# Optimization experiments

Measured on AMD Instinct MI355X. Metric: run time of the kernel, lower is better.

Reference implementation:

```python
import jax, jax.numpy as jnp
import numpy as np


def setup_inputs() -> dict:
    key = jax.random.key(0)
    ks = jax.random.split(key, 9)
    D, DK, DV = 512, 64, 64
    B, S = 4, 4096
    sd = 1.0 / np.sqrt(D).astype(np.float32)
    so = 1.0 / np.sqrt(DV).astype(np.float32)
    return {
        "x": jax.random.normal(ks[0], (B, S, D), dtype=jnp.float32),
        "Wq": jax.random.normal(ks[1], (D, DK), dtype=jnp.float32) * sd,
        "bq": jnp.zeros((DK,), dtype=jnp.float32),
        "Wk": jax.random.normal(ks[2], (D, DK), dtype=jnp.float32) * sd,
        "bk": jnp.zeros((DK,), dtype=jnp.float32),
        "Wv": jax.random.normal(ks[3], (D, DV), dtype=jnp.float32) * sd,
        "bv": jnp.zeros((DV,), dtype=jnp.float32),
        "Wo": jax.random.normal(ks[4], (DV, D), dtype=jnp.float32) * so,
        "bo": jnp.zeros((D,), dtype=jnp.float32),
    }


def reference(x, Wq, bq, Wk, bk, Wv, bv, Wo, bo):
    # x: (B, S, D)
    B, S, D = x.shape
    dk = Wq.shape[1]
    q = x @ Wq + bq            # (B, S, dk)
    k = x @ Wk + bk            # (B, S, dk)
    v = x @ Wv + bv            # (B, S, dv)
    scores = jnp.einsum("bik,bjk->bij", q, k) / jnp.sqrt(jnp.float32(dk))  # (B,S,S)
    # causal mask: True where j <= i (keep)
    causal = jnp.tril(jnp.ones((S, S), dtype=bool))
    scores = jnp.where(causal[None, :, :], scores, -jnp.inf)
    weights = jax.nn.softmax(scores, axis=-1)   # every row has >=1 unmasked entry
    out = jnp.einsum("bij,bjv->biv", weights, v)  # (B, S, dv)
    return out @ Wo + bo
```

## Files before the change

### kernel.cpp

```cpp
#include <hip/hip_runtime.h>
#include <hip/hip_bf16.h>

#define S_LEN 4096
#define D_MODEL 512
#define DKV 64
#define B_N 4
#define STR 72
#define VSTR 136

typedef __hip_bfloat16 bf16;
typedef __attribute__((ext_vector_type(8))) short short8;
typedef __attribute__((ext_vector_type(4))) float floatx4;

#define MFMA(a, b, c) __builtin_amdgcn_mfma_f32_16x16x32_bf16(a, b, c, 0, 0, 0)

__device__ __forceinline__ float b2f(bf16 v) { return __bfloat162float(v); }

__device__ __forceinline__ unsigned short f2bits(float v) {
    union { bf16 h; unsigned short u; } cv;
    cv.h = __float2bfloat16(v);
    return cv.u;
}
__device__ __forceinline__ float bits2f(unsigned short u) {
    union { bf16 h; unsigned short u; } cv;
    cv.u = u;
    return b2f(cv.h);
}

__global__ __launch_bounds__(64) void detect_kernel(const void* x, int* flag) {
    const int lane = threadIdx.x;
    const bf16* xb = (const bf16*)x;
    int bad = 0;
    for (int k = lane; k < 4096; k += 64) {
        float v = fabsf(b2f(xb[2 * k]));
        if (!(v < 64.f)) bad++;
    }
    #pragma unroll
    for (int off = 32; off >= 1; off >>= 1) bad += __shfl_xor(bad, off);
    if (lane == 0) *flag = (bad > 100) ? 1 : 0;
}

__global__ __launch_bounds__(512) void wprep_qkv_frag(
    const void* __restrict__ Wq, const void* __restrict__ bq,
    const void* __restrict__ Wk, const void* __restrict__ bk,
    const void* __restrict__ Wv, const void* __restrict__ bv,
    bf16* __restrict__ Wfh, bf16* __restrict__ Wfl, float* __restrict__ ball,
    const int* __restrict__ flag)
{
    __shared__ float xs[16][513];
    const int ct = blockIdx.x;
    const int c0 = ct * 16;
    const int g = c0 >> 6;
    const int cc0 = c0 & 63;
    const void* W    = (g == 0) ? Wq : (g == 1) ? Wk : Wv;
    const void* bias = (g == 0) ? bq : (g == 1) ? bk : bv;
    const int tid = threadIdx.x;
    const int f32 = *flag;

    #pragma unroll
    for (int i = 0; i < 16; ++i) {
        const int idx = tid + 512 * i;
        const int d = idx >> 4, j = idx & 15;
        const float v = f32 ? ((const float*)W)[(size_t)d * DKV + cc0 + j]
                            : b2f(((const bf16*)W)[(size_t)d * DKV + cc0 + j]);
        xs[j][d] = v;
    }
    __syncthreads();

    union Pack8 { uint4 u; unsigned short s[8]; };
    #pragma unroll
    for (int rep = 0; rep < 2; ++rep) {
        const int f = tid + rep * 512;
        const int kt = f >> 6, lane = f & 63;
        const int quad = lane >> 4, l15 = lane & 15;
        Pack8 ph, pl;
        #pragma unroll
        for (int j = 0; j < 8; ++j) {
            const float v = xs[l15][kt * 32 + quad * 8 + j];
            const unsigned short hb = f2bits(v);
            ph.s[j] = hb;
            pl.s[j] = f2bits(v - bits2f(hb));
        }
        const size_t o = (((size_t)ct * 16 + kt) * 64 + lane) * 8;
        *(uint4*)&Wfh[o] = ph.u;
        *(uint4*)&Wfl[o] = pl.u;
    }
    if (tid < 16)
        ball[c0 + tid] = f32 ? ((const float*)bias)[cc0 + tid]
                             : b2f(((const bf16*)bias)[cc0 + tid]);
}

__global__ __launch_bounds__(512) void wprep_o_frag(
    const void* __restrict__ Wo, const void* __restrict__ bo,
    bf16* __restrict__ WoFh, bf16* __restrict__ WoFl,
    float* __restrict__ ball2, const int* __restrict__ flag)
{
    __shared__ float ys[16][65];
    const int ctile = blockIdx.x;
    const int c0 = ctile * 16;
    const int tid = threadIdx.x;
    const int f32 = *flag;

    #pragma unroll
    for (int rep = 0; rep < 2; ++rep) {
        const int idx = tid + rep * 512;
        const int d = idx >> 4, j = idx & 15;
        const float v = f32 ? ((const float*)Wo)[(size_t)d * D_MODEL + c0 + j]
                            : b2f(((const bf16*)Wo)[(size_t)d * D_MODEL + c0 + j]);
        ys[j][d] = v;
    }
    __syncthreads();

    union Pack8 { uint4 u; unsigned short s[8]; };
    if (tid < 128) {
        const int kc = tid >> 6, lane = tid & 63;
        const int quad = lane >> 4, l15 = lane & 15;
        Pack8 ph, pl;
        #pragma unroll
        for (int j = 0; j < 8; ++j) {
            const float v = ys[l15][kc * 32 + quad * 8 + j];
            const unsigned short hb = f2bits(v);
            ph.s[j] = hb;
            pl.s[j] = f2bits(v - bits2f(hb));
        }
        const size_t o = (((size_t)ctile * 2 + kc) * 64 + lane) * 8;
        *(uint4*)&WoFh[o] = ph.u;
        *(uint4*)&WoFl[o] = pl.u;
    }
    if (tid < 16)
        ball2[c0 + tid] = f32 ? ((const float*)bo)[c0 + tid]
                              : b2f(((const bf16*)bo)[c0 + tid]);
}

__global__ __launch_bounds__(256) void qkv_mfma_bf16(
    const void* __restrict__ x,
    const bf16* __restrict__ Wfh, const float* __restrict__ ball,
    bf16* __restrict__ Qb, bf16* __restrict__ Kb, bf16* __restrict__ Vt,
    const int* __restrict__ flag)
{
    if (*flag) return;
    __shared__ unsigned short hiA[32 * D_MODEL];
    const int tid = threadIdx.x;
    const int rowBase = blockIdx.x * 32;

    const unsigned short* xr = (const unsigned short*)x + (size_t)rowBase * D_MODEL;
    #pragma unroll
    for (int i = 0; i < 8; ++i) {
        const int idx = tid + 256 * i;
        const int r = idx >> 6;
        const int c0 = (idx & 63) << 3;
        const uint4 hv = *(const uint4*)&xr[r * D_MODEL + c0];
        const int boff = (c0 * 2) ^ ((r & 7) << 4);
        *(uint4*)((char*)hiA + r * 1024 + boff) = hv;
    }
    __syncthreads();

    const int lane = tid & 63;
    const int w    = tid >> 6;
    const int quad = lane >> 4;
    const int l15  = lane & 15;
    const int wr   = w & 1;
    const int wcol = w >> 1;
    const int arow = wr * 16 + l15;
    const char* hib = (const char*)hiA + arow * 1024;
    const int swz = (arow & 7) << 4;

    floatx4 acc[6];
    #pragma unroll
    for (int ct = 0; ct < 6; ++ct) acc[ct] = (floatx4){0.f, 0.f, 0.f, 0.f};

    for (int kt = 0; kt < 16; ++kt) {
        const int boff = (kt * 64 + quad * 16) ^ swz;
        const short8 ah = *(const short8*)(hib + boff);
        #pragma unroll
        for (int ct = 0; ct < 6; ++ct) {
            const size_t fo = (((size_t)(wcol * 6 + ct) * 16 + kt) * 64 + lane) * 8;
            const short8 bh = *(const short8*)&Wfh[fo];
            acc[ct] = MFMA(ah, bh, acc[ct]);
        }
    }

    #pragma unroll
    for (int ct = 0; ct < 6; ++ct) {
        const int gc = wcol * 96 + ct * 16 + l15;
        const float bias = ball[gc];
        const float scale = (gc < 64) ? 0.18033688f : 1.0f;
        #pragma unroll
        for (int r = 0; r < 4; ++r) {
            const int gr = rowBase + wr * 16 + quad * 4 + r;
            const bf16 o = __float2bfloat16((acc[ct][r] + bias) * scale);
            if (gc < 64)       Qb[(size_t)gr * DKV + gc] = o;
            else if (gc < 128) Kb[(size_t)gr * DKV + (gc - 64)] = o;
            else {
                const int bb = gr >> 12, sidx = gr & (S_LEN - 1);
                Vt[((size_t)bb * DKV + (gc - 128)) * S_LEN + sidx] = o;
            }
        }
    }
}

__global__ __launch_bounds__(512) void qkv_mfma_f32(
    const void* __restrict__ x,
    const bf16* __restrict__ Wfh, const bf16* __restrict__ Wfl,
    const float* __restrict__ ball,
    bf16* __restrict__ Qb, bf16* __restrict__ Kb, bf16* __restrict__ Vt,
    const int* __restrict__ flag)
{
    if (!*flag) return;
    __shared__ unsigned short hiA[32 * D_MODEL];
    __shared__ unsigned short loA[32 * D_MODEL];
    const int tid = threadIdx.x;
    const int rowBase = blockIdx.x * 32;

    union Pack8 { uint4 u; unsigned short s[8]; };
    {
        const float* xr = (const float*)x + (size_t)rowBase * D_MODEL;
        #pragma unroll
        for (int i = 0; i < 4; ++i) {
            const int idx = tid + 512 * i;
            const int r = idx >> 6;
            const int c0 = (idx & 63) << 3;
            const float4 v0 = *(const float4*)&xr[r * D_MODEL + c0];
            const float4 v1 = *(const float4*)&xr[r * D_MODEL + c0 + 4];
            const float vv[8] = {v0.x, v0.y, v0.z, v0.w, v1.x, v1.y, v1.z, v1.w};
            Pack8 ph, pl;
            #pragma unroll
            for (int j = 0; j < 8; ++j) {
                const unsigned short hb = f2bits(vv[j]);
                ph.s[j] = hb;
                pl.s[j] = f2bits(vv[j] - bits2f(hb));
            }
            const int boff = (c0 * 2) ^ ((r & 7) << 4);
            *(uint4*)((char*)hiA + r * 1024 + boff) = ph.u;
            *(uint4*)((char*)loA + r * 1024 + boff) = pl.u;
        }
    }
    __syncthreads();

    const int lane = tid & 63;
    const int w    = tid >> 6;
    const int quad = lane >> 4;
    const int l15  = lane & 15;
    const int wr   = w & 1;
    const int wq   = w >> 1;
    const int arow = wr * 16 + l15;
    const char* hib = (const char*)hiA + arow * 1024;
    const char* lob = (const char*)loA + arow * 1024;
    const int swz = (arow & 7) << 4;

    floatx4 acc[3];
    #pragma unroll
    for (int ct = 0; ct < 3; ++ct) acc[ct] = (floatx4){0.f, 0.f, 0.f, 0.f};

    for (int kt = 0; kt < 16; ++kt) {
        const int boff = (kt * 64 + quad * 16) ^ swz;
        const short8 ah = *(const short8*)(hib + boff);
        const short8 al = *(const short8*)(lob + boff);
        #pragma unroll
        for (int ct = 0; ct < 3; ++ct) {
            const size_t fo = (((size_t)(wq * 3 + ct) * 16 + kt) * 64 + lane) * 8;
            const short8 bh = *(const short8*)&Wfh[fo];
            const short8 bl = *(const short8*)&Wfl[fo];
            acc[ct] = MFMA(ah, bh, acc[ct]);
            acc[ct] = MFMA(ah, bl, acc[ct]);
            acc[ct] = MFMA(al, bh, acc[ct]);
        }
    }

    #pragma unroll
    for (int ct = 0; ct < 3; ++ct) {
        const int gc = wq * 48 + ct * 16 + l15;
        const float bias = ball[gc];
        const float scale = (gc < 64) ? 0.18033688f : 1.0f;
        #pragma unroll
        for (int r = 0; r < 4; ++r) {
            const int gr = rowBase + wr * 16 + quad * 4 + r;
            const bf16 o = __float2bfloat16((acc[ct][r] + bias) * scale);
            if (gc < 64)       Qb[(size_t)gr * DKV + gc] = o;
            else if (gc < 128) Kb[(size_t)gr * DKV + (gc - 64)] = o;
            else {
                const int bb = gr >> 12, sidx = gr & (S_LEN - 1);
                Vt[((size_t)bb * DKV + (gc - 128)) * S_LEN + sidx] = o;
            }
        }
    }
}

__global__ __launch_bounds__(256, 3) void attn_mfma(
    const bf16* __restrict__ Qg, const bf16* __restrict__ Kg,
    const bf16* __restrict__ Vtg, float* __restrict__ Op,
    float* __restrict__ Mp, float* __restrict__ Lp, const int NS)
{
    const int bid = blockIdx.x;
    const int xcd = bid & 7;
    const int rest = bid >> 3;
    const int b   = xcd >> 1;
    const int khH = (NS == 4) ? (rest & 1) : 0;
    const int t64 = 63 - ((NS == 4) ? (rest >> 1) : rest);
    const int kh  = khH * 2 + (xcd & 1);
    const int rowBase = t64 * 64;
    const int tid = threadIdx.x;
    const int lane = tid & 63;
    const int w  = tid >> 6;
    const int quad = lane >> 4;
    const int l15  = lane & 15;

    __shared__ bf16 Kl[128 * STR];
    __shared__ bf16 Vl[64 * VSTR];
    __shared__ bf16 Pl[64 * VSTR];

    const bf16* Qb = Qg + ((size_t)b * S_LEN + rowBase) * DKV;
    const bf16* Kb = Kg + (size_t)b * S_LEN * DKV;
    const bf16* Vb = Vtg + (size_t)b * DKV * S_LEN;

    {
        const int qr = tid >> 2, qd = (tid & 3) * 16;
        *(uint4*)&Pl[qr * VSTR + qd]     = *(const uint4*)&Qb[qr * DKV + qd];
        *(uint4*)&Pl[qr * VSTR + qd + 8] = *(const uint4*)&Qb[qr * DKV + qd + 8];
    }
    __syncthreads();
    short8 qf0, qf1;
    {
        const int qoff = (w * 16 + l15) * VSTR + quad * 8;
        qf0 = *(const short8*)&Pl[qoff];
        qf1 = *(const short8*)&Pl[qoff + 32];
    }

    const short s1b = (short)0x3F80;
    const short8 ones = {s1b, s1b, s1b, s1b, s1b, s1b, s1b, s1b};

    floatx4 acc[4];
    #pragma unroll
    for (int v = 0; v < 4; ++v) acc[v] = (floatx4){0.f, 0.f, 0.f, 0.f};
    floatx4 accl = {0.f, 0.f, 0.f, 0.f};
    float m_run[4];
    #pragma unroll
    for (int r = 0; r < 4; ++r) m_run[r] = -1e30f;

    const int kbMax = (rowBase + 63) >> 7;
    const int kk = tid >> 1, dk = (tid & 1) * 32;
    const int vd = tid >> 2, vk = (tid & 3) * 32;

    uint4 kr0, kr1, kr2, kr3, vr0, vr1, vr2, vr3;
    int kb = kh;
    if (kb <= kbMax) {
        const uint4* ks = (const uint4*)&Kb[((size_t)(kb * 128 + kk)) * DKV + dk];
        kr0 = ks[0]; kr1 = ks[1]; kr2 = ks[2]; kr3 = ks[3];
        const uint4* vs = (const uint4*)&Vb[(size_t)vd * S_LEN + kb * 128 + vk];
        vr0 = vs[0]; vr1 = vs[1]; vr2 = vs[2]; vr3 = vs[3];
    }

    for (; kb <= kbMax; kb += NS) {
        __syncthreads();
        {
            uint4* kd = (uint4*)&Kl[kk * STR + dk];
            kd[0] = kr0; kd[1] = kr1; kd[2] = kr2; kd[3] = kr3;
            uint4* vdst = (uint4*)&Vl[vd * VSTR + vk];
            vdst[0] = vr0; vdst[1] = vr1; vdst[2] = vr2; vdst[3] = vr3;
        }
        __syncthreads();
        if (kb + NS <= kbMax) {
            const uint4* ks = (const uint4*)&Kb[((size_t)((kb + NS) * 128 + kk)) * DKV + dk];
            kr0 = ks[0]; kr1 = ks[1]; kr2 = ks[2]; kr3 = ks[3];
            const uint4* vs = (const uint4*)&Vb[(size_t)vd * S_LEN + (kb + NS) * 128 + vk];
            vr0 = vs[0]; vr1 = vs[1]; vr2 = vs[2]; vr3 = vs[3];
        }

        floatx4 s[8];
        #pragma unroll
        for (int jt = 0; jt < 8; ++jt) s[jt] = (floatx4){0.f, 0.f, 0.f, 0.f};
        {
            const int qk = quad * 8;
            #pragma unroll
            for (int jt = 0; jt < 8; ++jt) {
                const int kc = (jt * 16 + l15) * STR + qk;
                const short8 ba = *(const short8*)&Kl[kc];
                const short8 bb = *(const short8*)&Kl[kc + 32];
                s[jt] = MFMA(qf0, ba, s[jt]);
                s[jt] = MFMA(qf1, bb, s[jt]);
            }
        }
        if (kb == kbMax) {
            const int rowg = rowBase + w * 16 + quad * 4;
            #pragma unroll
            for (int jt = 0; jt < 8; ++jt) {
                const int kg = kb * 128 + jt * 16 + l15;
                #pragma unroll
                for (int r = 0; r < 4; ++r)
                    if (kg > rowg + r) s[jt][r] = -1e30f;
            }
        }
        float m4[4];
        #pragma unroll
        for (int r = 0; r < 4; ++r) {
            float mm = s[0][r];
            #pragma unroll
            for (int jt = 1; jt < 8; ++jt) mm = fmaxf(mm, s[jt][r]);
            m4[r] = mm;
        }
        #pragma unroll
        for (int off = 1; off < 16; off <<= 1) {
            #pragma unroll
            for (int r = 0; r < 4; ++r) m4[r] = fmaxf(m4[r], __shfl_xor(m4[r], off));
        }
        float alpha[4];
        #pragma unroll
        for (int r = 0; r < 4; ++r) {
            const float mnew = fmaxf(m_run[r], m4[r]);
            alpha[r] = exp2f(m_run[r] - mnew);
            m_run[r] = mnew;
        }
        #pragma unroll
        for (int r = 0; r < 4; ++r) {
            accl[r] *= alpha[r];
            #pragma unroll
            for (int v = 0; v < 4; ++v) acc[v][r] *= alpha[r];
            const int poff = (w * 16 + quad * 4 + r) * VSTR + l15;
            #pragma unroll
            for (int jt = 0; jt < 8; ++jt) {
                const float pp = exp2f(s[jt][r] - m_run[r]);
                Pl[poff + jt * 16] = __float2bfloat16(pp);
            }
        }
        asm volatile("s_waitcnt lgkmcnt(0)" ::: "memory");

        {
            const int pk = quad * 8;
            const int prow = (w * 16 + l15) * VSTR;
            short8 pa[4];
            #pragma unroll
            for (int c = 0; c < 4; ++c)
                pa[c] = *(const short8*)&Pl[prow + pk + c * 32];
            #pragma unroll
            for (int c = 0; c < 4; ++c) accl = MFMA(pa[c], ones, accl);
            #pragma unroll
            for (int v = 0; v < 4; ++v) {
                const int vrow = (v * 16 + l15) * VSTR;
                #pragma unroll
                for (int c = 0; c < 4; ++c) {
                    const short8 vb = *(const short8*)&Vl[vrow + pk + c * 32];
                    acc[v] = MFMA(pa[c], vb, acc[v]);
                }
            }
        }
    }
    #pragma unroll
    for (int r = 0; r < 4; ++r) {
        const int row = rowBase + w * 16 + quad * 4 + r;
        float* op = Op + (((size_t)kh * B_N + b) * S_LEN + row) * DKV + l15;
        #pragma unroll
        for (int v = 0; v < 4; ++v) op[v * 16] = acc[v][r];
    }
    if (l15 == 0) {
        #pragma unroll
        for (int r = 0; r < 4; ++r) {
            const int row = rowBase + w * 16 + quad * 4 + r;
            const size_t mi = ((size_t)kh * B_N + b) * S_LEN + row;
            Mp[mi] = m_run[r];
            Lp[mi] = accl[r];
        }
    }
}

#define PSTR 72
__global__ __launch_bounds__(256) void proj_mfma_bf16(
    const float* __restrict__ Op, const float* __restrict__ Mp,
    const float* __restrict__ Lp, const int NS,
    const bf16* __restrict__ WoFh, const float* __restrict__ ball2,
    bf16* __restrict__ out, const int* __restrict__ flag)
{
    if (*flag) return;
    __shared__ unsigned short Ah[32 * PSTR], Al[32 * PSTR];
    const int tid = threadIdx.x;
    const int rowBase = blockIdx.x * 32;

    {
        const int rr = tid >> 3, dd = (tid & 7) * 8;
        const int row = rowBase + rr;
        const size_t part = (size_t)B_N * S_LEN;
        float m = -1e30f;
        #pragma unroll 4
        for (int i = 0; i < NS; ++i) m = fmaxf(m, Mp[i * part + row]);
        float denom = 0.f;
        float oacc[8] = {0.f, 0.f, 0.f, 0.f, 0.f, 0.f, 0.f, 0.f};
        #pragma unroll 4
        for (int i = 0; i < NS; ++i) {
            const float wi = exp2f(Mp[i * part + row] - m);
            denom += Lp[i * part + row] * wi;
            const float* pi = Op + (i * part + row) * DKV + dd;
            #pragma unroll
            for (int j = 0; j < 8; ++j) oacc[j] += pi[j] * wi;
        }
        const float inv = 1.0f / denom;
        union Pack8 { uint4 u; unsigned short s[8]; };
        Pack8 ph, pl;
        #pragma unroll
        for (int j = 0; j < 8; ++j) {
            const float o = oacc[j] * inv;
            ph.s[j] = f2bits(o);
            pl.s[j] = f2bits(o - bits2f(ph.s[j]));
        }
        *(uint4*)&Ah[rr * PSTR + dd] = ph.u;
        *(uint4*)&Al[rr * PSTR + dd] = pl.u;
    }
    __syncthreads();

    const int lane = tid & 63;
    const int w    = tid >> 6;
    const int quad = lane >> 4;
    const int l15  = lane & 15;
    const int wr   = w & 1;
    const int wcq  = w >> 1;

    const int aoff = (wr * 16 + l15) * PSTR + quad * 8;
    const short8 ah0 = *(const short8*)&Ah[aoff];
    const short8 ah1 = *(const short8*)&Ah[aoff + 32];
    const short8 al0 = *(const short8*)&Al[aoff];
    const short8 al1 = *(const short8*)&Al[aoff + 32];

    floatx4 acc[16];
    #pragma unroll
    for (int ct = 0; ct < 16; ++ct) acc[ct] = (floatx4){0.f, 0.f, 0.f, 0.f};

    #pragma unroll
    for (int ct = 0; ct < 16; ++ct) {
        const int ctile = wcq * 16 + ct;
        const size_t o0 = (((size_t)ctile * 2 + 0) * 64 + lane) * 8;
        const size_t o1 = (((size_t)ctile * 2 + 1) * 64 + lane) * 8;
        const short8 bh0 = *(const short8*)&WoFh[o0];
        const short8 bh1 = *(const short8*)&WoFh[o1];
        acc[ct] = MFMA(ah0, bh0, acc[ct]);
        acc[ct] = MFMA(ah1, bh1, acc[ct]);
        acc[ct] = MFMA(al0, bh0, acc[ct]);
        acc[ct] = MFMA(al1, bh1, acc[ct]);
    }

    #pragma unroll
    for (int ct = 0; ct < 16; ++ct) {
        const int col = wcq * 256 + ct * 16 + l15;
        const float bias = ball2[col];
        #pragma unroll
        for (int r = 0; r < 4; ++r) {
            const int row = rowBase + wr * 16 + quad * 4 + r;
            out[(size_t)row * D_MODEL + col] = __float2bfloat16(acc[ct][r] + bias);
        }
    }
}

__global__ __launch_bounds__(512) void proj_mfma_f32(
    const float* __restrict__ Op, const float* __restrict__ Mp,
    const float* __restrict__ Lp, const int NS,
    const bf16* __restrict__ WoFh, const bf16* __restrict__ WoFl,
    const float* __restrict__ ball2, float* __restrict__ out,
    const int* __restrict__ flag)
{
    if (!*flag) return;
    __shared__ unsigned short Ah[32 * PSTR], Al[32 * PSTR];
    const int tid = threadIdx.x;
    const int rowBase = blockIdx.x * 32;

    {
        const int rr = tid >> 4, dd = (tid & 15) * 4;
        const int row = rowBase + rr;
        const size_t part = (size_t)B_N * S_LEN;
        float m = -1e30f;
        #pragma unroll 4
        for (int i = 0; i < NS; ++i) m = fmaxf(m, Mp[i * part + row]);
        float denom = 0.f;
        float oacc[4] = {0.f, 0.f, 0.f, 0.f};
        #pragma unroll 4
        for (int i = 0; i < NS; ++i) {
            const float wi = exp2f(Mp[i * part + row] - m);
            denom += Lp[i * part + row] * wi;
            const float4 v = *(const float4*)&Op[(i * part + row) * DKV + dd];
            oacc[0] += v.x * wi; oacc[1] += v.y * wi;
            oacc[2] += v.z * wi; oacc[3] += v.w * wi;
        }
        const float inv = 1.0f / denom;
        union Pack4 { uint2 u; unsigned short s[4]; };
        Pack4 ph, pl;
        #pragma unroll
        for (int j = 0; j < 4; ++j) {
            const float o = oacc[j] * inv;
            ph.s[j] = f2bits(o);
            pl.s[j] = f2bits(o - bits2f(ph.s[j]));
        }
        *(uint2*)&Ah[rr * PSTR + dd] = ph.u;
        *(uint2*)&Al[rr * PSTR + dd] = pl.u;
    }
    __syncthreads();

    const int lane = tid & 63;
    const int w    = tid >> 6;
    const int quad = lane >> 4;
    const int l15  = lane & 15;
    const int wr   = w & 1;
    const int wcq  = w >> 1;

    const int aoff = (wr * 16 + l15) * PSTR + quad * 8;
    const short8 ah0 = *(const short8*)&Ah[aoff];
    const short8 ah1 = *(const short8*)&Ah[aoff + 32];
    const short8 al0 = *(const short8*)&Al[aoff];
    const short8 al1 = *(const short8*)&Al[aoff + 32];

    floatx4 acc[8];
    #pragma unroll
    for (int ct = 0; ct < 8; ++ct) acc[ct] = (floatx4){0.f, 0.f, 0.f, 0.f};

    #pragma unroll
    for (int ct = 0; ct < 8; ++ct) {
        const int ctile = wcq * 8 + ct;
        const size_t o0 = (((size_t)ctile * 2 + 0) * 64 + lane) * 8;
        const size_t o1 = (((size_t)ctile * 2 + 1) * 64 + lane) * 8;
        const short8 bh0 = *(const short8*)&WoFh[o0];
        const short8 bh1 = *(const short8*)&WoFh[o1];
        const short8 bl0 = *(const short8*)&WoFl[o0];
        const short8 bl1 = *(const short8*)&WoFl[o1];
        acc[ct] = MFMA(ah0, bh0, acc[ct]);
        acc[ct] = MFMA(ah1, bh1, acc[ct]);
        acc[ct] = MFMA(ah0, bl0, acc[ct]);
        acc[ct] = MFMA(ah1, bl1, acc[ct]);
        acc[ct] = MFMA(al0, bh0, acc[ct]);
        acc[ct] = MFMA(al1, bh1, acc[ct]);
    }

    #pragma unroll
    for (int ct = 0; ct < 8; ++ct) {
        const int col = wcq * 128 + ct * 16 + l15;
        const float bias = ball2[col];
        #pragma unroll
        for (int r = 0; r < 4; ++r) {
            const int row = rowBase + wr * 16 + quad * 4 + r;
            out[(size_t)row * D_MODEL + col] = acc[ct][r] + bias;
        }
    }
}

extern "C" void kernel_launch(void* const* d_in, const int* in_sizes, int n_in,
                              void* d_out, int out_size, void* d_ws, size_t ws_size,
                              hipStream_t stream) {
    const void* x  = d_in[0];
    const void* Wq = d_in[1];
    const void* bq = d_in[2];
    const void* Wk = d_in[3];
    const void* bk = d_in[4];
    const void* Wv = d_in[5];
    const void* bv = d_in[6];
    const void* Wo = d_in[7];
    const void* bo = d_in[8];

    const int rows = B_N * S_LEN;
    const int NS = (ws_size >= (size_t)30 * 1024 * 1024) ? 4 : 2;

    char* p = (char*)d_ws;
    int*  flag = (int*)p;                          p += 256;
    bf16* Qb = (bf16*)p;                           p += (size_t)rows * DKV * 2;
    bf16* Kb = (bf16*)p;                           p += (size_t)rows * DKV * 2;
    bf16* Vt = (bf16*)p;                           p += (size_t)rows * DKV * 2;
    bf16* Wfh = (bf16*)p;                          p += (size_t)12 * 16 * 64 * 8 * 2;
    bf16* Wfl = (bf16*)p;                          p += (size_t)12 * 16 * 64 * 8 * 2;
    float* ball = (float*)p;                       p += 1024;
    bf16* WoFh = (bf16*)p;                         p += (size_t)32 * 2 * 64 * 8 * 2;
    bf16* WoFl = (bf16*)p;                         p += (size_t)32 * 2 * 64 * 8 * 2;
    float* ball2 = (float*)p;                      p += D_MODEL * 4;
    float* Op = (float*)p;                         p += (size_t)NS * rows * DKV * 4;
    float* Mp = (float*)p;                         p += (size_t)NS * rows * 4;
    float* Lp = (float*)p;                         p += (size_t)NS * rows * 4;

    detect_kernel<<<1, 64, 0, stream>>>(x, flag);
    wprep_qkv_frag<<<12, 512, 0, stream>>>(Wq, bq, Wk, bk, Wv, bv, Wfh, Wfl, ball, flag);
    wprep_o_frag<<<32, 512, 0, stream>>>(Wo, bo, WoFh, WoFl, ball2, flag);
    qkv_mfma_bf16<<<512, 256, 0, stream>>>(x, Wfh, ball, Qb, Kb, Vt, flag);
    qkv_mfma_f32<<<512, 512, 0, stream>>>(x, Wfh, Wfl, ball, Qb, Kb, Vt, flag);
    attn_mfma<<<256 * NS, 256, 0, stream>>>(Qb, Kb, Vt, Op, Mp, Lp, NS);
    proj_mfma_bf16<<<512, 256, 0, stream>>>(Op, Mp, Lp, NS, WoFh, ball2, (bf16*)d_out, flag);
    proj_mfma_f32<<<512, 512, 0, stream>>>(Op, Mp, Lp, NS, WoFh, WoFl, ball2, (float*)d_out, flag);
}
```

Measured before the change: 173.0 us.

## Merge dtype-variant kernels and enlarge attention query tile to 128 rows

Merges the two weight-prep kernels into one launch and folds the bf16/f32 variants of the QKV and output-projection kernels into single kernels that branch on the dtype flag. This removes several kernel launches, including early-exiting blocks. The attention kernel moves from 64 to 128 query rows per block with 512 threads, halving the grid and letting each K/V tile serve twice as many queries. The trade-off is coarser causal load balancing, a larger P buffer in shared memory, and lower occupancy.

```diff
diff --git a/kernel.cpp b/kernel.cpp
--- a/kernel.cpp
+++ b/kernel.cpp
@@ -40,180 +40,109 @@
     if (lane == 0) *flag = (bad > 100) ? 1 : 0;
 }
 
-__global__ __launch_bounds__(512) void wprep_qkv_frag(
+__global__ __launch_bounds__(512) void wprep_kernel(
     const void* __restrict__ Wq, const void* __restrict__ bq,
     const void* __restrict__ Wk, const void* __restrict__ bk,
     const void* __restrict__ Wv, const void* __restrict__ bv,
+    const void* __restrict__ Wo, const void* __restrict__ bo,
     bf16* __restrict__ Wfh, bf16* __restrict__ Wfl, float* __restrict__ ball,
+    bf16* __restrict__ WoFh, bf16* __restrict__ WoFl, float* __restrict__ ball2,
     const int* __restrict__ flag)
 {
     __shared__ float xs[16][513];
-    const int ct = blockIdx.x;
-    const int c0 = ct * 16;
-    const int g = c0 >> 6;
-    const int cc0 = c0 & 63;
-    const void* W    = (g == 0) ? Wq : (g == 1) ? Wk : Wv;
-    const void* bias = (g == 0) ? bq : (g == 1) ? bk : bv;
+    const int blk = blockIdx.x;
     const int tid = threadIdx.x;
     const int f32 = *flag;
-
-    #pragma unroll
-    for (int i = 0; i < 16; ++i) {
-        const int idx = tid + 512 * i;
-        const int d = idx >> 4, j = idx & 15;
-        const float v = f32 ? ((const float*)W)[(size_t)d * DKV + cc0 + j]
-                            : b2f(((const bf16*)W)[(size_t)d * DKV + cc0 + j]);
-        xs[j][d] = v;
-    }
-    __syncthreads();
-
     union Pack8 { uint4 u; unsigned short s[8]; };
-    #pragma unroll
-    for (int rep = 0; rep < 2; ++rep) {
-        const int f = tid + rep * 512;
-        const int kt = f >> 6, lane = f & 63;
-        const int quad = lane >> 4, l15 = lane & 15;
-        Pack8 ph, pl;
-        #pragma unroll
-        for (int j = 0; j < 8; ++j) {
-            const float v = xs[l15][kt * 32 + quad * 8 + j];
-            const unsigned short hb = f2bits(v);
-            ph.s[j] = hb;
-            pl.s[j] = f2bits(v - bits2f(hb));
-        }
-        const size_t o = (((size_t)ct * 16 + kt) * 64 + lane) * 8;
-        *(uint4*)&Wfh[o] = ph.u;
-        *(uint4*)&Wfl[o] = pl.u;
-    }
-    if (tid < 16)
-        ball[c0 + tid] = f32 ? ((const float*)bias)[cc0 + tid]
-                             : b2f(((const bf16*)bias)[cc0 + tid]);
-}
-
-__global__ __launch_bounds__(512) void wprep_o_frag(
-    const void* __restrict__ Wo, const void* __restrict__ bo,
-    bf16* __restrict__ WoFh, bf16* __restrict__ WoFl,
-    float* __restrict__ ball2, const int* __restrict__ flag)
-{
-    __shared__ float ys[16][65];
-    const int ctile = blockIdx.x;
-    const int c0 = ctile * 16;
-    const int tid = threadIdx.x;
-    const int f32 = *flag;
-
-    #pragma unroll
-    for (int rep = 0; rep < 2; ++rep) {
-        const int idx = tid + rep * 512;
-        const int d = idx >> 4, j = idx & 15;
-        const float v = f32 ? ((const float*)Wo)[(size_t)d * D_MODEL + c0 + j]
-                            : b2f(((const bf16*)Wo)[(size_t)d * D_MODEL + c0 + j]);
-        ys[j][d] = v;
-    }
-    __syncthreads();
-
-    union Pack8 { uint4 u; unsigned short s[8]; };
-    if (tid < 128) {
-        const int kc = tid >> 6, lane = tid & 63;
-        const int quad = lane >> 4, l15 = lane & 15;
-        Pack8 ph, pl;
-        #pragma unroll
-        for (int j = 0; j < 8; ++j) {
-            const float v = ys[l15][kc * 32 + quad * 8 + j];
-            const unsigned short hb = f2bits(v);
-            ph.s[j] = hb;
-            pl.s[j] = f2bits(v - bits2f(hb));
-        }
-        const size_t o = (((size_t)ctile * 2 + kc) * 64 + lane) * 8;
-        *(uint4*)&WoFh[o] = ph.u;
-        *(uint4*)&WoFl[o] = pl.u;
-    }
-    if (tid < 16)
-        ball2[c0 + tid] = f32 ? ((const float*)bo)[c0 + tid]
-                              : b2f(((const bf16*)bo)[c0 + tid]);
-}
-
-__global__ __launch_bounds__(256) void qkv_mfma_bf16(
-    const void* __restrict__ x,
-    const bf16* __restrict__ Wfh, const float* __restrict__ ball,
-    bf16* __restrict__ Qb, bf16* __restrict__ Kb, bf16* __restrict__ Vt,
-    const int* __restrict__ flag)
-{
-    if (*flag) return;
-    __shared__ unsigned short hiA[32 * D_MODEL];
-    const int tid = threadIdx.x;
-    const int rowBase = blockIdx.x * 32;
-
-    const unsigned short* xr = (const unsigned short*)x + (size_t)rowBase * D_MODEL;
-    #pragma unroll
-    for (int i = 0; i < 8; ++i) {
-        const int idx = tid + 256 * i;
-        const int r = idx >> 6;
-        const int c0 = (idx & 63) << 3;
-        const uint4 hv = *(const uint4*)&xr[r * D_MODEL + c0];
-        const int boff = (c0 * 2) ^ ((r & 7) << 4);
-        *(uint4*)((char*)hiA + r * 1024 + boff) = hv;
-    }
-    __syncthreads();
-
-    const int lane = tid & 63;
-    const int w    = tid >> 6;
-    const int quad = lane >> 4;
-    const int l15  = lane & 15;
-    const int wr   = w & 1;
-    const int wcol = w >> 1;
-    const int arow = wr * 16 + l15;
-    const char* hib = (const char*)hiA + arow * 1024;
-    const int swz = (arow & 7) << 4;
-
-    floatx4 acc[6];
-    #pragma unroll
-    for (int ct = 0; ct < 6; ++ct) acc[ct] = (floatx4){0.f, 0.f, 0.f, 0.f};
-
-    for (int kt = 0; kt < 16; ++kt) {
-        const int boff = (kt * 64 + quad * 16) ^ swz;
-        const short8 ah = *(const short8*)(hib + boff);
-        #pragma unroll
-        for (int ct = 0; ct < 6; ++ct) {
-            const size_t fo = (((size_t)(wcol * 6 + ct) * 16 + kt) * 64 + lane) * 8;
-            const short8 bh = *(const short8*)&Wfh[fo];
-            acc[ct] = MFMA(ah, bh, acc[ct]);
-        }
-    }
-
-    #pragma unroll
-    for (int ct = 0; ct < 6; ++ct) {
-        const int gc = wcol * 96 + ct * 16 + l15;
-        const float bias = ball[gc];
-        const float scale = (gc < 64) ? 0.18033688f : 1.0f;
-        #pragma unroll
-        for (int r = 0; r < 4; ++r) {
-            const int gr = rowBase + wr * 16 + quad * 4 + r;
-            const bf16 o = __float2bfloat16((acc[ct][r] + bias) * scale);
-            if (gc < 64)       Qb[(size_t)gr * DKV + gc] = o;
-            else if (gc < 128) Kb[(size_t)gr * DKV + (gc - 64)] = o;
-            else {
-                const int bb = gr >> 12, sidx = gr & (S_LEN - 1);
-                Vt[((size_t)bb * DKV + (gc - 128)) * S_LEN + sidx] = o;
-            }
-        }
-    }
-}
-
-__global__ __launch_bounds__(512) void qkv_mfma_f32(
+
+    if (blk < 12) {
+        const int ct = blk;
+        const int c0 = ct * 16;
+        const int g = c0 >> 6;
+        const int cc0 = c0 & 63;
+        const void* W    = (g == 0) ? Wq : (g == 1) ? Wk : Wv;
+        const void* bias = (g == 0) ? bq : (g == 1) ? bk : bv;
+
+        #pragma unroll
+        for (int i = 0; i < 16; ++i) {
+            const int idx = tid + 512 * i;
+            const int d = idx >> 4, j = idx & 15;
+            const float v = f32 ? ((const float*)W)[(size_t)d * DKV + cc0 + j]
+                                : b2f(((const bf16*)W)[(size_t)d * DKV + cc0 + j]);
+            xs[j][d] = v;
+        }
+        __syncthreads();
+
+        #pragma unroll
+        for (int rep = 0; rep < 2; ++rep) {
+            const int f = tid + rep * 512;
+            const int kt = f >> 6, lane = f & 63;
+            const int quad = lane >> 4, l15 = lane & 15;
+            Pack8 ph, pl;
+            #pragma unroll
+            for (int j = 0; j < 8; ++j) {
+                const float v = xs[l15][kt * 32 + quad * 8 + j];
+                const unsigned short hb = f2bits(v);
+                ph.s[j] = hb;
+                pl.s[j] = f2bits(v - bits2f(hb));
+            }
+            const size_t o = (((size_t)ct * 16 + kt) * 64 + lane) * 8;
+            *(uint4*)&Wfh[o] = ph.u;
+            *(uint4*)&Wfl[o] = pl.u;
+        }
+        if (tid < 16)
+            ball[c0 + tid] = f32 ? ((const float*)bias)[cc0 + tid]
+                                 : b2f(((const bf16*)bias)[cc0 + tid]);
+    } else {
+        const int ctile = blk - 12;
+        const int c0 = ctile * 16;
+
+        #pragma unroll
+        for (int rep = 0; rep < 2; ++rep) {
+            const int idx = tid + rep * 512;
+            const int d = idx >> 4, j = idx & 15;
+            const float v = f32 ? ((const float*)Wo)[(size_t)d * D_MODEL + c0 + j]
+                                : b2f(((const bf16*)Wo)[(size_t)d * D_MODEL + c0 + j]);
+            xs[j][d] = v;
+        }
+        __syncthreads();
+
+        if (tid < 128) {
+            const int kc = tid >> 6, lane = tid & 63;
+            const int quad = lane >> 4, l15 = lane & 15;
+            Pack8 ph, pl;
+            #pragma unroll
+            for (int j = 0; j < 8; ++j) {
+                const float v = xs[l15][kc * 32 + quad * 8 + j];
+                const unsigned short hb = f2bits(v);
+                ph.s[j] = hb;
+                pl.s[j] = f2bits(v - bits2f(hb));
+            }
+            const size_t o = (((size_t)ctile * 2 + kc) * 64 + lane) * 8;
+            *(uint4*)&WoFh[o] = ph.u;
+            *(uint4*)&WoFl[o] = pl.u;
+        }
+        if (tid < 16)
+            ball2[c0 + tid] = f32 ? ((const float*)bo)[c0 + tid]
+                                  : b2f(((const bf16*)bo)[c0 + tid]);
+    }
+}
+
+__global__ __launch_bounds__(512) void qkv_mfma(
     const void* __restrict__ x,
     const bf16* __restrict__ Wfh, const bf16* __restrict__ Wfl,
     const float* __restrict__ ball,
     bf16* __restrict__ Qb, bf16* __restrict__ Kb, bf16* __restrict__ Vt,
     const int* __restrict__ flag)
 {
-    if (!*flag) return;
     __shared__ unsigned short hiA[32 * D_MODEL];
     __shared__ unsigned short loA[32 * D_MODEL];
     const int tid = threadIdx.x;
     const int rowBase = blockIdx.x * 32;
+    const int f32 = *flag;
 
     union Pack8 { uint4 u; unsigned short s[8]; };
-    {
+    if (f32) {
         const float* xr = (const float*)x + (size_t)rowBase * D_MODEL;
         #pragma unroll
         for (int i = 0; i < 4; ++i) {
@@ -233,6 +162,17 @@
             const int boff = (c0 * 2) ^ ((r & 7) << 4);
             *(uint4*)((char*)hiA + r * 1024 + boff) = ph.u;
             *(uint4*)((char*)loA + r * 1024 + boff) = pl.u;
+        }
+    } else {
+        const unsigned short* xr = (const unsigned short*)x + (size_t)rowBase * D_MODEL;
+        #pragma unroll
+        for (int i = 0; i < 4; ++i) {
+            const int idx = tid + 512 * i;
+            const int r = idx >> 6;
+            const int c0 = (idx & 63) << 3;
+            const uint4 hv = *(const uint4*)&xr[r * D_MODEL + c0];
+            const int boff = (c0 * 2) ^ ((r & 7) << 4);
+            *(uint4*)((char*)hiA + r * 1024 + boff) = hv;
         }
     }
     __syncthreads();
@@ -252,18 +192,31 @@
     #pragma unroll
     for (int ct = 0; ct < 3; ++ct) acc[ct] = (floatx4){0.f, 0.f, 0.f, 0.f};
 
-    for (int kt = 0; kt < 16; ++kt) {
-        const int boff = (kt * 64 + quad * 16) ^ swz;
-        const short8 ah = *(const short8*)(hib + boff);
-        const short8 al = *(const short8*)(lob + boff);
-        #pragma unroll
-        for (int ct = 0; ct < 3; ++ct) {
-            const size_t fo = (((size_t)(wq * 3 + ct) * 16 + kt) * 64 + lane) * 8;
-            const short8 bh = *(const short8*)&Wfh[fo];
-            const short8 bl = *(const short8*)&Wfl[fo];
-            acc[ct] = MFMA(ah, bh, acc[ct]);
-            acc[ct] = MFMA(ah, bl, acc[ct]);
-            acc[ct] = MFMA(al, bh, acc[ct]);
+    if (f32) {
+        for (int kt = 0; kt < 16; ++kt) {
+            const int boff = (kt * 64 + quad * 16) ^ swz;
+            const short8 ah = *(const short8*)(hib + boff);
+            const short8 al = *(const short8*)(lob + boff);
+            #pragma unroll
+            for (int ct = 0; ct < 3; ++ct) {
+                const size_t fo = (((size_t)(wq * 3 + ct) * 16 + kt) * 64 + lane) * 8;
+                const short8 bh = *(const short8*)&Wfh[fo];
+                const short8 bl = *(const short8*)&Wfl[fo];
+                acc[ct] = MFMA(ah, bh, acc[ct]);
+                acc[ct] = MFMA(ah, bl, acc[ct]);
+                acc[ct] = MFMA(al, bh, acc[ct]);
+            }
+        }
+    } else {
+        for (int kt = 0; kt < 16; ++kt) {
+            const int boff = (kt * 64 + quad * 16) ^ swz;
+            const short8 ah = *(const short8*)(hib + boff);
+            #pragma unroll
+            for (int ct = 0; ct < 3; ++ct) {
+                const size_t fo = (((size_t)(wq * 3 + ct) * 16 + kt) * 64 + lane) * 8;
+                const short8 bh = *(const short8*)&Wfh[fo];
+                acc[ct] = MFMA(ah, bh, acc[ct]);
+            }
         }
     }
 
@@ -286,7 +239,7 @@
     }
 }
 
-__global__ __launch_bounds__(256, 3) void attn_mfma(
+__global__ __launch_bounds__(512, 2) void attn_mfma(
     const bf16* __restrict__ Qg, const bf16* __restrict__ Kg,
     const bf16* __restrict__ Vtg, float* __restrict__ Op,
     float* __restrict__ Mp, float* __restrict__ Lp, const int NS)
@@ -296,9 +249,9 @@
     const int rest = bid >> 3;
     const int b   = xcd >> 1;
     const int khH = (NS == 4) ? (rest & 1) : 0;
-    const int t64 = 63 - ((NS == 4) ? (rest >> 1) : rest);
+    const int t   = 31 - ((NS == 4) ? (rest >> 1) : rest);
     const int kh  = khH * 2 + (xcd & 1);
-    const int rowBase = t64 * 64;
+    const int rowBase = t * 128;
     const int tid = threadIdx.x;
     const int lane = tid & 63;
     const int w  = tid >> 6;
@@ -307,7 +260,7 @@
 
     __shared__ bf16 Kl[128 * STR];
     __shared__ bf16 Vl[64 * VSTR];
-    __shared__ bf16 Pl[64 * VSTR];
+    __shared__ bf16 Pl[128 * VSTR];
 
     const bf16* Qb = Qg + ((size_t)b * S_LEN + rowBase) * DKV;
     const bf16* Kb = Kg + (size_t)b * S_LEN * DKV;
@@ -337,33 +290,33 @@
     #pragma unroll
     for (int r = 0; r < 4; ++r) m_run[r] = -1e30f;
 
-    const int kbMax = (rowBase + 63) >> 7;
-    const int kk = tid >> 1, dk = (tid & 1) * 32;
-    const int vd = tid >> 2, vk = (tid & 3) * 32;
-
-    uint4 kr0, kr1, kr2, kr3, vr0, vr1, vr2, vr3;
+    const int kbMax = t;
+    const int kk = tid >> 2, dk = (tid & 3) * 16;
+    const int vd = tid >> 3, vk = (tid & 7) * 16;
+
+    uint4 kr0, kr1, vr0, vr1;
     int kb = kh;
     if (kb <= kbMax) {
         const uint4* ks = (const uint4*)&Kb[((size_t)(kb * 128 + kk)) * DKV + dk];
-        kr0 = ks[0]; kr1 = ks[1]; kr2 = ks[2]; kr3 = ks[3];
+        kr0 = ks[0]; kr1 = ks[1];
         const uint4* vs = (const uint4*)&Vb[(size_t)vd * S_LEN + kb * 128 + vk];
-        vr0 = vs[0]; vr1 = vs[1]; vr2 = vs[2]; vr3 = vs[3];
+        vr0 = vs[0]; vr1 = vs[1];
     }
 
     for (; kb <= kbMax; kb += NS) {
         __syncthreads();
         {
             uint4* kd = (uint4*)&Kl[kk * STR + dk];
-            kd[0] = kr0; kd[1] = kr1; kd[2] = kr2; kd[3] = kr3;
+            kd[0] = kr0; kd[1] = kr1;
             uint4* vdst = (uint4*)&Vl[vd * VSTR + vk];
-            vdst[0] = vr0; vdst[1] = vr1; vdst[2] = vr2; vdst[3] = vr3;
+            vdst[0] = vr0; vdst[1] = vr1;
         }
         __syncthreads();
         if (kb + NS <= kbMax) {
             const uint4* ks = (const uint4*)&Kb[((size_t)((kb + NS) * 128 + kk)) * DKV + dk];
-            kr0 = ks[0]; kr1 = ks[1]; kr2 = ks[2]; kr3 = ks[3];
+            kr0 = ks[0]; kr1 = ks[1];
             const uint4* vs = (const uint4*)&Vb[(size_t)vd * S_LEN + (kb + NS) * 128 + vk];
-            vr0 = vs[0]; vr1 = vs[1]; vr2 = vs[2]; vr3 = vs[3];
+            vr0 = vs[0]; vr1 = vs[1];
         }
 
         floatx4 s[8];
@@ -463,101 +416,17 @@
 }
 
 #define PSTR 72
-__global__ __launch_bounds__(256) void proj_mfma_bf16(
+__global__ __launch_bounds__(512) void proj_mfma(
     const float* __restrict__ Op, const float* __restrict__ Mp,
     const float* __restrict__ Lp, const int NS,
-    const bf16* __restrict__ WoFh, const float* __restrict__ ball2,
-    bf16* __restrict__ out, const int* __restrict__ flag)
+    const bf16* __restrict__ WoFh, const bf16* __restrict__ WoFl,
+    const float* __restrict__ ball2, void* __restrict__ out,
+    const int* __restrict__ flag)
 {
-    if (*flag) return;
     __shared__ unsigned short Ah[32 * PSTR], Al[32 * PSTR];
     const int tid = threadIdx.x;
     const int rowBase = blockIdx.x * 32;
-
-    {
-        const int rr = tid >> 3, dd = (tid & 7) * 8;
-        const int row = rowBase + rr;
-        const size_t part = (size_t)B_N * S_LEN;
-        float m = -1e30f;
-        #pragma unroll 4
-        for (int i = 0; i < NS; ++i) m = fmaxf(m, Mp[i * part + row]);
-        float denom = 0.f;
-        float oacc[8] = {0.f, 0.f, 0.f, 0.f, 0.f, 0.f, 0.f, 0.f};
-        #pragma unroll 4
-        for (int i = 0; i < NS; ++i) {
-            const float wi = exp2f(Mp[i * part + row] - m);
-            denom += Lp[i * part + row] * wi;
-            const float* pi = Op + (i * part + row) * DKV + dd;
-            #pragma unroll
-            for (int j = 0; j < 8; ++j) oacc[j] += pi[j] * wi;
-        }
-        const float inv = 1.0f / denom;
-        union Pack8 { uint4 u; unsigned short s[8]; };
-        Pack8 ph, pl;
-        #pragma unroll
-        for (int j = 0; j < 8; ++j) {
-            const float o = oacc[j] * inv;
-            ph.s[j] = f2bits(o);
-            pl.s[j] = f2bits(o - bits2f(ph.s[j]));
-        }
-        *(uint4*)&Ah[rr * PSTR + dd] = ph.u;
-        *(uint4*)&Al[rr * PSTR + dd] = pl.u;
-    }
-    __syncthreads();
-
-    const int lane = tid & 63;
-    const int w    = tid >> 6;
-    const int quad = lane >> 4;
-    const int l15  = lane & 15;
-    const int wr   = w & 1;
-    const int wcq  = w >> 1;
-
-    const int aoff = (wr * 16 + l15) * PSTR + quad * 8;
-    const short8 ah0 = *(const short8*)&Ah[aoff];
-    const short8 ah1 = *(const short8*)&Ah[aoff + 32];
-    const short8 al0 = *(const short8*)&Al[aoff];
-    const short8 al1 = *(const short8*)&Al[aoff + 32];
-
-    floatx4 acc[16];
-    #pragma unroll
-    for (int ct = 0; ct < 16; ++ct) acc[ct] = (floatx4){0.f, 0.f, 0.f, 0.f};
-
-    #pragma unroll
-    for (int ct = 0; ct < 16; ++ct) {
-        const int ctile = wcq * 16 + ct;
-        const size_t o0 = (((size_t)ctile * 2 + 0) * 64 + lane) * 8;
-        const size_t o1 = (((size_t)ctile * 2 + 1) * 64 + lane) * 8;
-        const short8 bh0 = *(const short8*)&WoFh[o0];
-        const short8 bh1 = *(const short8*)&WoFh[o1];
-        acc[ct] = MFMA(ah0, bh0, acc[ct]);
-        acc[ct] = MFMA(ah1, bh1, acc[ct]);
-        acc[ct] = MFMA(al0, bh0, acc[ct]);
-        acc[ct] = MFMA(al1, bh1, acc[ct]);
-    }
-
-    #pragma unroll
-    for (int ct = 0; ct < 16; ++ct) {
-        const int col = wcq * 256 + ct * 16 + l15;
-        const float bias = ball2[col];
-        #pragma unroll
-        for (int r = 0; r < 4; ++r) {
-            const int row = rowBase + wr * 16 + quad * 4 + r;
-            out[(size_t)row * D_MODEL + col] = __float2bfloat16(acc[ct][r] + bias);
-        }
-    }
-}
-
-__global__ __launch_bounds__(512) void proj_mfma_f32(
-    const float* __restrict__ Op, const float* __restrict__ Mp,
-    const float* __restrict__ Lp, const int NS,
-    const bf16* __restrict__ WoFh, const bf16* __restrict__ WoFl,
-    const float* __restrict__ ball2, float* __restrict__ out,
-    const int* __restrict__ flag)
-{
-    if (!*flag) return;
-    __shared__ unsigned short Ah[32 * PSTR], Al[32 * PSTR];
-    const int tid = threadIdx.x;
-    const int rowBase = blockIdx.x * 32;
+    const int f32 = *flag;
 
     {
         const int rr = tid >> 4, dd = (tid & 15) * 4;
@@ -607,31 +476,57 @@
     #pragma unroll
     for (int ct = 0; ct < 8; ++ct) acc[ct] = (floatx4){0.f, 0.f, 0.f, 0.f};
 
-    #pragma unroll
-    for (int ct = 0; ct < 8; ++ct) {
-        const int ctile = wcq * 8 + ct;
-        const size_t o0 = (((size_t)ctile * 2 + 0) * 64 + lane) * 8;
-        const size_t o1 = (((size_t)ctile * 2 + 1) * 64 + lane) * 8;
-        const short8 bh0 = *(const short8*)&WoFh[o0];
-        const short8 bh1 = *(const short8*)&WoFh[o1];
-        const short8 bl0 = *(const short8*)&WoFl[o0];
-        const short8 bl1 = *(const short8*)&WoFl[o1];
-        acc[ct] = MFMA(ah0, bh0, acc[ct]);
-        acc[ct] = MFMA(ah1, bh1, acc[ct]);
-        acc[ct] = MFMA(ah0, bl0, acc[ct]);
-        acc[ct] = MFMA(ah1, bl1, acc[ct]);
-        acc[ct] = MFMA(al0, bh0, acc[ct]);
-        acc[ct] = MFMA(al1, bh1, acc[ct]);
-    }
-
-    #pragma unroll
-    for (int ct = 0; ct < 8; ++ct) {
-        const int col = wcq * 128 + ct * 16 + l15;
-        const float bias = ball2[col];
-        #pragma unroll
-        for (int r = 0; r < 4; ++r) {
-            const int row = rowBase + wr * 16 + quad * 4 + r;
-            out[(size_t)row * D_MODEL + col] = acc[ct][r] + bias;
+    if (f32) {
+        #pragma unroll
+        for (int ct = 0; ct < 8; ++ct) {
+            const int ctile = wcq * 8 + ct;
+            const size_t o0 = (((size_t)ctile * 2 + 0) * 64 + lane) * 8;
+            const size_t o1 = (((size_t)ctile * 2 + 1) * 64 + lane) * 8;
+            const short8 bh0 = *(const short8*)&WoFh[o0];
+            const short8 bh1 = *(const short8*)&WoFh[o1];
+            const short8 bl0 = *(const short8*)&WoFl[o0];
+            const short8 bl1 = *(const short8*)&WoFl[o1];
+            acc[ct] = MFMA(ah0, bh0, acc[ct]);
+            acc[ct] = MFMA(ah1, bh1, acc[ct]);
+            acc[ct] = MFMA(ah0, bl0, acc[ct]);
+            acc[ct] = MFMA(ah1, bl1, acc[ct]);
+            acc[ct] = MFMA(al0, bh0, acc[ct]);
+            acc[ct] = MFMA(al1, bh1, acc[ct]);
+        }
+        float* outf = (float*)out;
+        #pragma unroll
+        for (int ct = 0; ct < 8; ++ct) {
+            const int col = wcq * 128 + ct * 16 + l15;
+            const float bias = ball2[col];
+            #pragma unroll
+            for (int r = 0; r < 4; ++r) {
+                const int row = rowBase + wr * 16 + quad * 4 + r;
+                outf[(size_t)row * D_MODEL + col] = acc[ct][r] + bias;
+            }
+        }
+    } else {
+        #pragma unroll
+        for (int ct = 0; ct < 8; ++ct) {
+            const int ctile = wcq * 8 + ct;
+            const size_t o0 = (((size_t)ctile * 2 + 0) * 64 + lane) * 8;
+            const size_t o1 = (((size_t)ctile * 2 + 1) * 64 + lane) * 8;
+            const short8 bh0 = *(const short8*)&WoFh[o0];
+            const short8 bh1 = *(const short8*)&WoFh[o1];
+            acc[ct] = MFMA(ah0, bh0, acc[ct]);
+            acc[ct] = MFMA(ah1, bh1, acc[ct]);
+            acc[ct] = MFMA(al0, bh0, acc[ct]);
+            acc[ct] = MFMA(al1, bh1, acc[ct]);
+        }
+        bf16* outb = (bf16*)out;
+        #pragma unroll
+        for (int ct = 0; ct < 8; ++ct) {
+            const int col = wcq * 128 + ct * 16 + l15;
+            const float bias = ball2[col];
+            #pragma unroll
+            for (int r = 0; r < 4; ++r) {
+                const int row = rowBase + wr * 16 + quad * 4 + r;
+                outb[(size_t)row * D_MODEL + col] = __float2bfloat16(acc[ct][r] + bias);
+            }
         }
     }
 }
@@ -668,11 +563,9 @@
     float* Lp = (float*)p;                         p += (size_t)NS * rows * 4;
 
     detect_kernel<<<1, 64, 0, stream>>>(x, flag);
-    wprep_qkv_frag<<<12, 512, 0, stream>>>(Wq, bq, Wk, bk, Wv, bv, Wfh, Wfl, ball, flag);
-    wprep_o_frag<<<32, 512, 0, stream>>>(Wo, bo, WoFh, WoFl, ball2, flag);
-    qkv_mfma_bf16<<<512, 256, 0, stream>>>(x, Wfh, ball, Qb, Kb, Vt, flag);
-    qkv_mfma_f32<<<512, 512, 0, stream>>>(x, Wfh, Wfl, ball, Qb, Kb, Vt, flag);
-    attn_mfma<<<256 * NS, 256, 0, stream>>>(Qb, Kb, Vt, Op, Mp, Lp, NS);
-    proj_mfma_bf16<<<512, 256, 0, stream>>>(Op, Mp, Lp, NS, WoFh, ball2, (bf16*)d_out, flag);
-    proj_mfma_f32<<<512, 512, 0, stream>>>(Op, Mp, Lp, NS, WoFh, WoFl, ball2, (float*)d_out, flag);
-}
+    wprep_kernel<<<44, 512, 0, stream>>>(Wq, bq, Wk, bk, Wv, bv, Wo, bo,
+                                         Wfh, Wfl, ball, WoFh, WoFl, ball2, flag);
+    qkv_mfma<<<512, 512, 0, stream>>>(x, Wfh, Wfl, ball, Qb, Kb, Vt, flag);
+    attn_mfma<<<128 * NS, 512, 0, stream>>>(Qb, Kb, Vt, Op, Mp, Lp, NS);
+    proj_mfma<<<512, 512, 0, stream>>>(Op, Mp, Lp, NS, WoFh, WoFl, ball2, d_out, flag);
+}
```

Measured after the change: 169.9 us (median of 2 runs). No clear change (-1.8%).
